# Kernel optimization log

Measured on AMD Instinct MI355X. Metric: run time of the kernel, lower is better.

The kernel has to match this reference:

```python
import jax, jax.numpy as jnp
import numpy as np

WIN_H, WIN_W = 8, 16
N = WIN_H * WIN_W            # 128 tokens per window
DIM, HEADS = 512, 16
TOW = 64 // WIN_H            # type_of_windows = input_resolution[0] // window_size[0] = 8
B_WIN = 2048                 # number of windows (B_)


def _earth_position_index():
    # Faithful port of get_earth_position_index (torch wraps negative indices;
    # we pre-wrap with mod so the gather uses nonnegative indices identically).
    ch = np.arange(WIN_H)
    cw = np.arange(WIN_W)
    coords = np.stack(np.meshgrid(ch, cw, indexing='ij'))        # [2, h, w]
    cf = coords.reshape(2, -1)                                   # [2, N]
    rel = cf[:, :, None] - cf[:, None, :]                        # [2, N, N]
    rel = rel.transpose(1, 2, 0).copy()                          # [N, N, 2]
    rel[:, :, 0] *= 2 * WIN_W - 1
    rel[:, :, 1] += WIN_W - 1
    idx = rel.sum(-1)                                            # [N, N], may be negative
    table_len = WIN_H ** 2 * (2 * WIN_W - 1)                     # 1984
    return (idx % table_len).astype(np.int32)


def setup_inputs() -> dict:
    key = jax.random.key(0)
    ks = jax.random.split(key, 6)
    table_len = WIN_H ** 2 * (2 * WIN_W - 1)
    inv_sqrt_dim = 1.0 / np.sqrt(DIM)
    return {
        'x': jax.random.normal(ks[0], (B_WIN, N, DIM), dtype=jnp.float32),
        'qkv_w': jax.random.normal(ks[1], (3 * DIM, DIM), dtype=jnp.float32) * inv_sqrt_dim,
        'qkv_b': jax.random.normal(ks[2], (3 * DIM,), dtype=jnp.float32) * 0.02,
        'proj_w': jax.random.normal(ks[3], (DIM, DIM), dtype=jnp.float32) * inv_sqrt_dim,
        'proj_b': jax.random.normal(ks[4], (DIM,), dtype=jnp.float32) * 0.02,
        'bias_table': jax.random.normal(ks[5], (table_len, TOW, HEADS), dtype=jnp.float32) * 0.02,
        'pos_index': jnp.asarray(_earth_position_index()),
    }


def reference(x, qkv_w, qkv_b, proj_w, proj_b, bias_table, pos_index):
    B_, Nn, C = x.shape
    hd = C // HEADS
    scale = hd ** (-0.5)
    # fused QKV projection: [B_, N, 3, H, hd]
    qkv = (x @ qkv_w.T + qkv_b).reshape(B_, Nn, 3, HEADS, hd)
    q = qkv[:, :, 0].transpose(0, 2, 1, 3) * scale               # [B_, H, N, hd]
    k = qkv[:, :, 1].transpose(0, 2, 1, 3)
    v = qkv[:, :, 2].transpose(0, 2, 1, 3)
    attn = jnp.einsum('bhnd,bhmd->bhnm', q, k)                   # [B_, H, N, N]
    # earth position bias: gather [N*N] rows -> [N, N, TOW, H], pick middle latitude
    epb = bias_table[pos_index.reshape(-1)].reshape(Nn, Nn, TOW, HEADS)
    epb = epb[:, :, TOW // 2, :]                                 # [N, N, H]
    attn = attn + epb.transpose(2, 0, 1)[None]                   # + [1, H, N, N]
    attn = jax.nn.softmax(attn, axis=-1)
    out = jnp.einsum('bhnm,bhmd->bhnd', attn, v)                 # [B_, H, N, hd]
    out = out.transpose(0, 2, 1, 3).reshape(B_, Nn, C)
    return out @ proj_w.T + proj_b
```

## Files before the change

### kernel.cpp

```cpp
#include <hip/hip_runtime.h>
#include <hip/hip_bf16.h>


typedef short short8 __attribute__((ext_vector_type(8)));
typedef float f32x4 __attribute__((ext_vector_type(4)));
typedef unsigned short u16;
typedef unsigned int u32;

__device__ __forceinline__ u16 f2bf(float f) {
    __bf16 h = (__bf16)f;
    union { __bf16 b; u16 u; } v; v.b = h;
    return v.u;
}

__device__ __forceinline__ f32x4 mfma16(short8 a, short8 b, f32x4 c) {
    return __builtin_amdgcn_mfma_f32_16x16x32_bf16(a, b, c, 0, 0, 0);
}

#define GLDS16(gsrc, ldst)                                                  \
    __builtin_amdgcn_global_load_lds(                                       \
        (const __attribute__((address_space(1))) void*)(gsrc),              \
        (__attribute__((address_space(3))) void*)(ldst), 16, 0, 0)

__global__ __launch_bounds__(256) void cvt_x_kernel(
    const float4* __restrict__ xin, int4* __restrict__ xbf)
{
    int idx = blockIdx.x * 256 + threadIdx.x;
    for (; idx < 16777216; idx += 8192 * 256) {
        const float4 a = xin[idx * 2], b = xin[idx * 2 + 1];
        int4 o;
        o.x = (u32)f2bf(a.x) | ((u32)f2bf(a.y) << 16);
        o.y = (u32)f2bf(a.z) | ((u32)f2bf(a.w) << 16);
        o.z = (u32)f2bf(b.x) | ((u32)f2bf(b.y) << 16);
        o.w = (u32)f2bf(b.z) | ((u32)f2bf(b.w) << 16);
        xbf[idx] = o;
    }
}

__global__ __launch_bounds__(256) void prep_kernel(
    const float* __restrict__ qkv_w, const float* __restrict__ proj_w,
    const float* __restrict__ btab, const int* __restrict__ pidx,
    u16* __restrict__ qkvw_bf, u16* __restrict__ projw_bf,
    float* __restrict__ epb)
{
    const int i = blockIdx.x * 256 + threadIdx.x;
    qkvw_bf[i] = f2bf(qkv_w[i]);
    if (i < 512 * 512) projw_bf[i] = f2bf(proj_w[i]);
    if (i < 16 * 128 * 128) {
        const int rc = i & 16383, h = i >> 14;
        epb[i] = btab[pidx[rc] * 128 + 64 + h];
    }
}


template<bool EPI_QKV>
__global__ __launch_bounds__(256) void gemm_bt(
    const u16* __restrict__ A, const u16* __restrict__ Bt,
    const float* __restrict__ bias, void* __restrict__ Cv,
    u16* __restrict__ kb, u16* __restrict__ vb,
    const int Nn, const int K, const float qscale)
{
    __shared__ __attribute__((aligned(16))) char sm[32768];
    char* As = sm;
    char* Bs = sm + 16384;

    const int tid = threadIdx.x;
    const int lane = tid & 63;
    const int w = tid >> 6;
    const int lo = lane & 15, g = lane >> 4;
    const int wm = w >> 1, wn = w & 1;
    const int wofs = __builtin_amdgcn_readfirstlane(w) * 1024;
    const int ntile = Nn >> 7;

    int wg = blockIdx.x;
    {
        const int cpx = gridDim.x >> 3;
        wg = (wg & 7) * cpx + (wg >> 3);
    }
    const int bm = wg / ntile, bn = wg % ntile;
    const size_t m0 = (size_t)bm << 7;
    const int n0 = bn << 7;
    const int nk = K >> 6;

    const u16* pa[4];
    const u16* pb[4];
#pragma unroll
    for (int i = 0; i < 4; ++i) {
        const int s = i * 256 + tid;
        const int r = s >> 3, c16 = s & 7;
        const int csw = (c16 ^ (r & 7)) << 3;
        pa[i] = A + (m0 + r) * (size_t)K + csw;
        pb[i] = Bt + (size_t)(n0 + r) * K + csw;
    }

#define STAGE(kt)                                                          \
    do {                                                                   \
        const int koff = (kt) * 64;                                        \
        _Pragma("unroll")                                                  \
        for (int i = 0; i < 4; ++i)                                        \
            GLDS16(pa[i] + koff, As + i * 4096 + wofs);                    \
        _Pragma("unroll")                                                  \
        for (int i = 0; i < 4; ++i)                                        \
            GLDS16(pb[i] + koff, Bs + i * 4096 + wofs);                    \
    } while (0)

    f32x4 acc[4][4] = {};

    STAGE(0);
    for (int kt = 0;;) {
        __syncthreads();
#pragma unroll
        for (int kk = 0; kk < 2; ++kk) {
            short8 af[4], bq[4];
            const int cb = (kk * 4 + g) << 4;
            const int sz = (lo & 7) << 4;
#pragma unroll
            for (int i = 0; i < 4; ++i) {
                const int ra = wm * 64 + i * 16 + lo;
                af[i] = *(const short8*)(As + ((ra * 128 + cb) ^ sz));
                const int rb = wn * 64 + i * 16 + lo;
                bq[i] = *(const short8*)(Bs + ((rb * 128 + cb) ^ sz));
            }
#pragma unroll
            for (int i = 0; i < 4; ++i)
#pragma unroll
                for (int j = 0; j < 4; ++j)
                    acc[i][j] = mfma16(af[i], bq[j], acc[i][j]);
        }
        if (++kt == nk) break;
        __syncthreads();
        STAGE(kt);
    }
#undef STAGE

    if constexpr (EPI_QKV) {
        __syncthreads();
        u16* Ct = (u16*)sm;
        const int b16 = ((int)(m0 >> 7)) * 16;
        const int tsel = bn >> 2;
        const int h0 = (bn & 3) << 2;
        u16* outb = (tsel == 0) ? (u16*)Cv : (tsel == 1) ? kb : vb;
        const float sc = (tsel == 0) ? qscale : 1.0f;
#pragma unroll
        for (int j = 0; j < 4; ++j) {
            const int c = wn * 64 + j * 16 + lo;
            const float bv = bias[n0 + c];
#pragma unroll
            for (int i = 0; i < 4; ++i)
#pragma unroll
                for (int ii = 0; ii < 4; ++ii) {
                    const int r = wm * 64 + i * 16 + g * 4 + ii;
                    Ct[r * 128 + c] = f2bf((acc[i][j][ii] + bv) * sc);
                }
        }
        __syncthreads();
#pragma unroll
        for (int it = 0; it < 8; ++it) {
            const int idx = it * 256 + tid;
            const int r = idx >> 4, s2 = idx & 15;
            const int hl = s2 >> 2, d0 = (s2 & 3) * 8;
            *(int4*)(outb + ((size_t)(b16 + h0 + hl) * 128 + r) * 32 + d0) =
                *(const int4*)(Ct + r * 128 + s2 * 8);
        }
    } else {
        float* Cg = (float*)Cv;
#pragma unroll
        for (int j = 0; j < 4; ++j) {
            const int c = wn * 64 + j * 16 + lo;
            const float bv = bias[n0 + c];
#pragma unroll
            for (int i = 0; i < 4; ++i)
#pragma unroll
                for (int ii = 0; ii < 4; ++ii) {
                    const size_t r = m0 + wm * 64 + i * 16 + g * 4 + ii;
                    Cg[r * (size_t)Nn + n0 + c] = acc[i][j][ii] + bv;
                }
        }
    }
}

__global__ __launch_bounds__(256) void attn_kernel(
    const u16* __restrict__ qbuf, const u16* __restrict__ kbuf,
    const u16* __restrict__ vbuf, const float* __restrict__ epb,
    u16* __restrict__ aout)
{
    __shared__ __attribute__((aligned(16))) char smem[43520];
    u16 (*Vt)[136]      = (u16(*)[136])smem;
    char* Qs            = smem + 8704;
    char* Ks            = smem + 16896;
    u16 (*Ps)[32][136]  = (u16(*)[32][136])(smem + 8704);
    u16 (*Os)[32]       = (u16(*)[32])smem;

    const int h = blockIdx.x >> 11;
    const int b = blockIdx.x & 2047;
    const int tid = threadIdx.x;
    const int lane = tid & 63, w = tid >> 6;
    const int lo = lane & 15, g = lane >> 4;
    const int wu = __builtin_amdgcn_readfirstlane(w);

    const size_t hb = (size_t)(b * 16 + h) * 4096;
    const u16* qp = qbuf + hb;
    const u16* kp = kbuf + hb;
    const u16* vp = vbuf + hb;

    const int c8 = ((lane & 3) ^ ((lane >> 3) & 3)) * 8;
    const int rofs = (lane >> 2) * 32;
#pragma unroll
    for (int cc = 0; cc < 2; ++cc) {
        const int ch = wu * 2 + cc;
        GLDS16(qp + ch * 512 + rofs + c8, Qs + ch * 1024);
        GLDS16(kp + ch * 512 + rofs + c8, Ks + ch * 1024);
    }
#pragma unroll
    for (int it = 0; it < 2; ++it) {
        const int idx = tid + it * 256;
        const int n = idx >> 2, d8 = (idx & 3) * 8;
        union { int4 q; u16 u[8]; } vu;
        vu.q = *(const int4*)(vp + n * 32 + d8);
#pragma unroll
        for (int j = 0; j < 8; ++j) Vt[d8 + j][n] = vu.u[j];
    }
    __syncthreads();

    const int r0 = w * 32;
    const int csw16 = (g ^ ((lo >> 1) & 3)) << 4;

    short8 aq[2], bk[8];
    aq[0] = *(const short8*)(Qs + (r0 + lo) * 64 + csw16);
    aq[1] = *(const short8*)(Qs + (r0 + 16 + lo) * 64 + csw16);
#pragma unroll
    for (int j = 0; j < 8; ++j)
        bk[j] = *(const short8*)(Ks + (j * 16 + lo) * 64 + csw16);

    f32x4 acc[2][8];
#pragma unroll
    for (int j = 0; j < 8; ++j) {
        f32x4 z = {0.f, 0.f, 0.f, 0.f};
        acc[0][j] = mfma16(aq[0], bk[j], z);
        acc[1][j] = mfma16(aq[1], bk[j], z);
    }

    const float* eb = epb + (h << 14);
    float mrow[2][4], rsum[2][4];
#pragma unroll
    for (int mt = 0; mt < 2; ++mt)
#pragma unroll
        for (int ii = 0; ii < 4; ++ii) { mrow[mt][ii] = -1e30f; rsum[mt][ii] = 0.f; }

#pragma unroll
    for (int mt = 0; mt < 2; ++mt)
#pragma unroll
        for (int j = 0; j < 8; ++j)
#pragma unroll
            for (int ii = 0; ii < 4; ++ii) {
                const int r = r0 + mt * 16 + g * 4 + ii;
                const int c = j * 16 + lo;
                const float sv = acc[mt][j][ii] + eb[(r << 7) + c];
                acc[mt][j][ii] = sv;
                mrow[mt][ii] = fmaxf(mrow[mt][ii], sv);
            }
#pragma unroll
    for (int d = 1; d < 16; d <<= 1)
#pragma unroll
        for (int mt = 0; mt < 2; ++mt)
#pragma unroll
            for (int ii = 0; ii < 4; ++ii)
                mrow[mt][ii] = fmaxf(mrow[mt][ii], __shfl_xor(mrow[mt][ii], d, 64));

    __syncthreads();

#pragma unroll
    for (int mt = 0; mt < 2; ++mt)
#pragma unroll
        for (int j = 0; j < 8; ++j)
#pragma unroll
            for (int ii = 0; ii < 4; ++ii) {
                const float p = __expf(acc[mt][j][ii] - mrow[mt][ii]);
                rsum[mt][ii] += p;
                Ps[w][mt * 16 + g * 4 + ii][j * 16 + lo] = f2bf(p);
            }
#pragma unroll
    for (int d = 1; d < 16; d <<= 1)
#pragma unroll
        for (int mt = 0; mt < 2; ++mt)
#pragma unroll
            for (int ii = 0; ii < 4; ++ii)
                rsum[mt][ii] += __shfl_xor(rsum[mt][ii], d, 64);

    f32x4 o[2][2] = {};
#pragma unroll
    for (int kk = 0; kk < 4; ++kk) {
        short8 av[2];
        av[0] = *(const short8*)(&Ps[w][lo][kk * 32 + g * 8]);
        av[1] = *(const short8*)(&Ps[w][16 + lo][kk * 32 + g * 8]);
#pragma unroll
        for (int dt = 0; dt < 2; ++dt) {
            const short8 bv = *(const short8*)(&Vt[dt * 16 + lo][kk * 32 + g * 8]);
            o[0][dt] = mfma16(av[0], bv, o[0][dt]);
            o[1][dt] = mfma16(av[1], bv, o[1][dt]);
        }
    }

    __syncthreads();

#pragma unroll
    for (int mt = 0; mt < 2; ++mt)
#pragma unroll
        for (int dt = 0; dt < 2; ++dt)
#pragma unroll
            for (int ii = 0; ii < 4; ++ii)
                Os[r0 + mt * 16 + g * 4 + ii][dt * 16 + lo] =
                    f2bf(o[mt][dt][ii] / rsum[mt][ii]);
    __syncthreads();

    u16* op = aout + (size_t)b * 128 * 512 + h * 32;
#pragma unroll
    for (int it = 0; it < 2; ++it) {
        const int idx = tid + it * 256;
        const int r = idx >> 2, c = (idx & 3) * 8;
        *(int4*)(op + (size_t)r * 512 + c) = *(const int4*)(&Os[r][c]);
    }
}

extern "C" void kernel_launch(void* const* d_in, const int* in_sizes, int n_in,
                              void* d_out, int out_size, void* d_ws, size_t ws_size,
                              hipStream_t stream)
{
    const float* x      = (const float*)d_in[0];
    const float* qkv_w  = (const float*)d_in[1];
    const float* qkv_b  = (const float*)d_in[2];
    const float* proj_w = (const float*)d_in[3];
    const float* proj_b = (const float*)d_in[4];
    const float* btab   = (const float*)d_in[5];
    const int*   pidx   = (const int*)d_in[6];

    char* ws = (char*)d_ws;
    u16*   xbf      = (u16*)(ws);
    u16*   attnbuf  = (u16*)(ws);
    u16*   qkvw_bf  = (u16*)(ws + 268435456);
    u16*   projw_bf = (u16*)(ws + 270008320);
    float* epb      = (float*)(ws + 270532608);
    u16*   qbuf     = (u16*)(ws + 271581184);
    u16*   kbuf     = (u16*)(ws + 540016640);
    u16*   vbuf     = (u16*)(ws + 808452096);

    const float qscale = 0.17677669529663687f;

    cvt_x_kernel<<<dim3(8192), dim3(256), 0, stream>>>(
        (const float4*)x, (int4*)xbf);

    prep_kernel<<<dim3(3072), dim3(256), 0, stream>>>(
        qkv_w, proj_w, btab, pidx, qkvw_bf, projw_bf, epb);

    gemm_bt<true><<<dim3(2048 * 12), dim3(256), 0, stream>>>(
        xbf, qkvw_bf, qkv_b, qbuf, kbuf, vbuf, 1536, 512, qscale);

    attn_kernel<<<dim3(32768), dim3(256), 0, stream>>>(
        qbuf, kbuf, vbuf, epb, attnbuf);

    gemm_bt<false><<<dim3(2048 * 4), dim3(256), 0, stream>>>(
        attnbuf, projw_bf, proj_b, d_out, nullptr, nullptr, 512, 512, 1.0f);
}
```

Before: 1.287 ms.

## Halve GEMM K-tile, swap MFMA operands for transposed-output vector epilogue

The GEMM K-step drops from 64 to 32, halving LDS to 16KB with a new XOR swizzle and one MFMA round per step. The MFMA operands are swapped so each lane holds four consecutive output columns. That lets the epilogue write packed bf16x4 or float4 directly to global memory, dropping the LDS staging pass and two barriers in the QKV path. The change trades twice as many sync and load rounds per K for higher occupancy and cheaper, vectorized stores.

```diff
diff --git a/kernel.cpp b/kernel.cpp
--- a/kernel.cpp
+++ b/kernel.cpp
@@ -60,9 +60,7 @@
     u16* __restrict__ kb, u16* __restrict__ vb,
     const int Nn, const int K, const float qscale)
 {
-    __shared__ __attribute__((aligned(16))) char sm[32768];
-    char* As = sm;
-    char* Bs = sm + 16384;
+    __shared__ __attribute__((aligned(16))) char sm[16384];
 
     const int tid = threadIdx.x;
     const int lane = tid & 63;
@@ -80,53 +78,44 @@
     const int bm = wg / ntile, bn = wg % ntile;
     const size_t m0 = (size_t)bm << 7;
     const int n0 = bn << 7;
-    const int nk = K >> 6;
-
-    const u16* pa[4];
-    const u16* pb[4];
-#pragma unroll
-    for (int i = 0; i < 4; ++i) {
-        const int s = i * 256 + tid;
-        const int r = s >> 3, c16 = s & 7;
-        const int csw = (c16 ^ (r & 7)) << 3;
-        pa[i] = A + (m0 + r) * (size_t)K + csw;
-        pb[i] = Bt + (size_t)(n0 + r) * K + csw;
-    }
+    const int nk = K >> 5;
+
+    const int rs = w * 16 + (lane >> 2);
+    const int c8 = ((lane & 3) ^ ((lane >> 3) & 3)) * 8;
+    const u16* pa0 = A + (m0 + rs) * (size_t)K + c8;
+    const u16* pa1 = pa0 + (size_t)64 * K;
+    const u16* pb0 = Bt + (size_t)(n0 + rs) * K + c8;
+    const u16* pb1 = pb0 + (size_t)64 * K;
 
 #define STAGE(kt)                                                          \
     do {                                                                   \
-        const int koff = (kt) * 64;                                        \
-        _Pragma("unroll")                                                  \
-        for (int i = 0; i < 4; ++i)                                        \
-            GLDS16(pa[i] + koff, As + i * 4096 + wofs);                    \
-        _Pragma("unroll")                                                  \
-        for (int i = 0; i < 4; ++i)                                        \
-            GLDS16(pb[i] + koff, Bs + i * 4096 + wofs);                    \
+        const int ko = (kt) << 5;                                          \
+        char* d = sm + wofs;                                               \
+        GLDS16(pa0 + ko, d);                                               \
+        GLDS16(pa1 + ko, d + 4096);                                        \
+        GLDS16(pb0 + ko, d + 8192);                                        \
+        GLDS16(pb1 + ko, d + 12288);                                       \
     } while (0)
 
     f32x4 acc[4][4] = {};
+
+    const int csw16 = (g ^ ((lo >> 1) & 3)) << 4;
 
     STAGE(0);
     for (int kt = 0;;) {
         __syncthreads();
-#pragma unroll
-        for (int kk = 0; kk < 2; ++kk) {
-            short8 af[4], bq[4];
-            const int cb = (kk * 4 + g) << 4;
-            const int sz = (lo & 7) << 4;
-#pragma unroll
-            for (int i = 0; i < 4; ++i) {
-                const int ra = wm * 64 + i * 16 + lo;
-                af[i] = *(const short8*)(As + ((ra * 128 + cb) ^ sz));
-                const int rb = wn * 64 + i * 16 + lo;
-                bq[i] = *(const short8*)(Bs + ((rb * 128 + cb) ^ sz));
-            }
-#pragma unroll
-            for (int i = 0; i < 4; ++i)
-#pragma unroll
-                for (int j = 0; j < 4; ++j)
-                    acc[i][j] = mfma16(af[i], bq[j], acc[i][j]);
+        short8 af[4], bq[4];
+#pragma unroll
+        for (int i = 0; i < 4; ++i) {
+            af[i] = *(const short8*)(sm + (wm * 64 + i * 16 + lo) * 64 + csw16);
+            bq[i] = *(const short8*)(sm + 8192
+                                     + (wn * 64 + i * 16 + lo) * 64 + csw16);
         }
+#pragma unroll
+        for (int i = 0; i < 4; ++i)
+#pragma unroll
+            for (int j = 0; j < 4; ++j)
+                acc[i][j] = mfma16(bq[j], af[i], acc[i][j]);
         if (++kt == nk) break;
         __syncthreads();
         STAGE(kt);
@@ -134,8 +123,6 @@
 #undef STAGE
 
     if constexpr (EPI_QKV) {
-        __syncthreads();
-        u16* Ct = (u16*)sm;
         const int b16 = ((int)(m0 >> 7)) * 16;
         const int tsel = bn >> 2;
         const int h0 = (bn & 3) << 2;
@@ -143,38 +130,37 @@
         const float sc = (tsel == 0) ? qscale : 1.0f;
 #pragma unroll
         for (int j = 0; j < 4; ++j) {
-            const int c = wn * 64 + j * 16 + lo;
-            const float bv = bias[n0 + c];
-#pragma unroll
-            for (int i = 0; i < 4; ++i)
-#pragma unroll
-                for (int ii = 0; ii < 4; ++ii) {
-                    const int r = wm * 64 + i * 16 + g * 4 + ii;
-                    Ct[r * 128 + c] = f2bf((acc[i][j][ii] + bv) * sc);
-                }
-        }
-        __syncthreads();
-#pragma unroll
-        for (int it = 0; it < 8; ++it) {
-            const int idx = it * 256 + tid;
-            const int r = idx >> 4, s2 = idx & 15;
-            const int hl = s2 >> 2, d0 = (s2 & 3) * 8;
-            *(int4*)(outb + ((size_t)(b16 + h0 + hl) * 128 + r) * 32 + d0) =
-                *(const int4*)(Ct + r * 128 + s2 * 8);
+            const int nn = wn * 64 + j * 16 + g * 4;
+            const float4 bv = *(const float4*)(bias + n0 + nn);
+            const int hl = nn >> 5, d0 = nn & 31;
+#pragma unroll
+            for (int i = 0; i < 4; ++i) {
+                const size_t m = wm * 64 + i * 16 + lo;
+                uint2 pk;
+                pk.x = (u32)f2bf((acc[i][j][0] + bv.x) * sc)
+                     | ((u32)f2bf((acc[i][j][1] + bv.y) * sc) << 16);
+                pk.y = (u32)f2bf((acc[i][j][2] + bv.z) * sc)
+                     | ((u32)f2bf((acc[i][j][3] + bv.w) * sc) << 16);
+                *(uint2*)(outb + ((size_t)(b16 + h0 + hl) * 128 + m) * 32 + d0)
+                    = pk;
+            }
         }
     } else {
         float* Cg = (float*)Cv;
 #pragma unroll
         for (int j = 0; j < 4; ++j) {
-            const int c = wn * 64 + j * 16 + lo;
-            const float bv = bias[n0 + c];
-#pragma unroll
-            for (int i = 0; i < 4; ++i)
-#pragma unroll
-                for (int ii = 0; ii < 4; ++ii) {
-                    const size_t r = m0 + wm * 64 + i * 16 + g * 4 + ii;
-                    Cg[r * (size_t)Nn + n0 + c] = acc[i][j][ii] + bv;
-                }
+            const int nn = wn * 64 + j * 16 + g * 4;
+            const float4 bv = *(const float4*)(bias + n0 + nn);
+#pragma unroll
+            for (int i = 0; i < 4; ++i) {
+                const size_t m = m0 + wm * 64 + i * 16 + lo;
+                float4 v;
+                v.x = acc[i][j][0] + bv.x;
+                v.y = acc[i][j][1] + bv.y;
+                v.z = acc[i][j][2] + bv.z;
+                v.w = acc[i][j][3] + bv.w;
+                *(float4*)(Cg + m * (size_t)Nn + n0 + nn) = v;
+            }
         }
     }
 }
```

Measured after the change: 1.393 ms, median of 4. +8.2%, slower.
